# Optimization experiments

Hardware: AMD Instinct MI355X
Metric: run time of the kernel (lower is better)

The kernel has to match this reference:

```python
import jax, jax.numpy as jnp
import numpy as np

DEPTH = 9
SIGMA = 0.1
IN_SIGMA = 1.0
TOTAL_VARS = 2 ** DEPTH - 2  # 510 = sum of 2^(depth-d-1) for d in [0, depth-2]


def setup_inputs() -> dict:
    key = jax.random.key(0)
    N = 262144
    eps = jax.random.normal(key, (N, TOTAL_VARS), dtype=jnp.float32)
    return {"eps": eps, "N": N}


def reference(eps, N):
    # Collider binary tree sampling, vectorized per level.
    # Level d has 2^(DEPTH-d-1) variables; each variable's mean is the
    # join (sum) of a consecutive pair of parents from the previous level.
    outs = []
    offset = 0
    prev = None
    for d in range(DEPTH - 1):
        width = 2 ** (DEPTH - d - 1)
        e = jax.lax.dynamic_slice_in_dim(eps, offset, width, axis=1)  # [N, width]
        offset += width
        if d == 0:
            # root-level leaves: zero mean, in_sigma scale
            x = IN_SIGMA * e
        else:
            # join_link(parent_2k, parent_2k+1) = sum of adjacent pair
            m = prev[:, 0::2] + prev[:, 1::2]  # [N, width]
            x = m + SIGMA * e
        outs.append(x)
        prev = x
    # Flat level-major layout, same ordering as torch samples_list concatenated.
    return jnp.concatenate(outs, axis=1)  # [N, TOTAL_VARS]
```

## Files before the change

kernel.cpp:

```cpp
#include <hip/hip_runtime.h>


#define TOTAL_VARS 510
#define SIGMA 0.1f

__global__ __launch_bounds__(256) void collider_kernel(
    const float* __restrict__ eps,
    float* __restrict__ out,
    int N)
{
    const int wid  = (int)((blockIdx.x * blockDim.x + threadIdx.x) >> 6);
    const int lane = (int)(threadIdx.x & 63);
    if (wid >= N) return;

    const float* __restrict__ ep = eps + (size_t)wid * TOTAL_VARS;
    float* __restrict__ op = out + (size_t)wid * TOTAL_VARS;

    const float2 a01 = *reinterpret_cast<const float2*>(ep + 4 * lane);
    const float2 a23 = *reinterpret_cast<const float2*>(ep + 4 * lane + 2);
    *reinterpret_cast<float2*>(op + 4 * lane)     = a01;
    *reinterpret_cast<float2*>(op + 4 * lane + 2) = a23;

    const float2 e1 = *reinterpret_cast<const float2*>(ep + 256 + 2 * lane);
    const float x1a = a01.x + a01.y + SIGMA * e1.x;
    const float x1b = a23.x + a23.y + SIGMA * e1.y;
    float2 o1; o1.x = x1a; o1.y = x1b;
    *reinterpret_cast<float2*>(op + 256 + 2 * lane) = o1;

    const float e2 = ep[384 + lane];
    const float x2 = x1a + x1b + SIGMA * e2;
    op[384 + lane] = x2;

    float prev = x2;
#pragma unroll
    for (int d = 3; d < 8; ++d) {
        const int w   = 256 >> d;
        const int off = 512 - (512 >> d);
        const float a = __shfl(prev, 2 * lane);
        const float b = __shfl(prev, 2 * lane + 1);
        float e = 0.0f;
        if (lane < w) e = ep[off + lane];
        const float v = a + b + SIGMA * e;
        if (lane < w) op[off + lane] = v;
        prev = v;
    }
}

extern "C" void kernel_launch(void* const* d_in, const int* in_sizes, int n_in,
                              void* d_out, int out_size, void* d_ws, size_t ws_size,
                              hipStream_t stream) {
    const float* eps = (const float*)d_in[0];
    float* out = (float*)d_out;
    const int N = in_sizes[0] / TOTAL_VARS;

    const int threads = 256;
    const int rows_per_block = threads / 64;
    const int blocks = (N + rows_per_block - 1) / rows_per_block;
    collider_kernel<<<blocks, threads, 0, stream>>>(eps, out, N);
}
```

Baseline: 197.9 us.

## Stage 8-row blocks through LDS with coalesced float4 global loads and stores

Each block now copies 8 contiguous rows (4080 floats) from global memory into LDS using aligned float4 loads, computes the tree levels in LDS with two rows per wave, then writes the block back with float4 stores. This replaces the per-row float2 and scalar global accesses, which are misaligned because the row stride is 510 floats, with fully coalesced 16-byte transfers. In exchange it adds about 16KB of LDS per block, two barriers, and a launch that assumes N is divisible by 8 with no tail guard.

```diff
diff --git a/kernel.cpp b/kernel.cpp
--- a/kernel.cpp
+++ b/kernel.cpp
@@ -2,6 +2,9 @@
 
 
 #define TOTAL_VARS 510
+#define ROWS_PER_BLOCK 8
+#define BLOCK_FLOATS (ROWS_PER_BLOCK * TOTAL_VARS)
+#define BLOCK_F4     (BLOCK_FLOATS / 4)
 #define SIGMA 0.1f
 
 __global__ __launch_bounds__(256) void collider_kernel(
@@ -9,40 +12,61 @@
     float* __restrict__ out,
     int N)
 {
-    const int wid  = (int)((blockIdx.x * blockDim.x + threadIdx.x) >> 6);
-    const int lane = (int)(threadIdx.x & 63);
-    if (wid >= N) return;
+    __shared__ __align__(16) float lds[BLOCK_FLOATS];
 
-    const float* __restrict__ ep = eps + (size_t)wid * TOTAL_VARS;
-    float* __restrict__ op = out + (size_t)wid * TOTAL_VARS;
+    const int tid = (int)threadIdx.x;
+    const size_t base = (size_t)blockIdx.x * BLOCK_FLOATS;
 
-    const float2 a01 = *reinterpret_cast<const float2*>(ep + 4 * lane);
-    const float2 a23 = *reinterpret_cast<const float2*>(ep + 4 * lane + 2);
-    *reinterpret_cast<float2*>(op + 4 * lane)     = a01;
-    *reinterpret_cast<float2*>(op + 4 * lane + 2) = a23;
+    const float4* __restrict__ gin = reinterpret_cast<const float4*>(eps + base);
+    float4* l4 = reinterpret_cast<float4*>(lds);
+#pragma unroll
+    for (int i = 0; i < 4; ++i) {
+        const int idx = tid + i * 256;
+        if (idx < BLOCK_F4) l4[idx] = gin[idx];
+    }
+    __syncthreads();
 
-    const float2 e1 = *reinterpret_cast<const float2*>(ep + 256 + 2 * lane);
-    const float x1a = a01.x + a01.y + SIGMA * e1.x;
-    const float x1b = a23.x + a23.y + SIGMA * e1.y;
-    float2 o1; o1.x = x1a; o1.y = x1b;
-    *reinterpret_cast<float2*>(op + 256 + 2 * lane) = o1;
+    const int wave = tid >> 6;
+    const int lane = tid & 63;
 
-    const float e2 = ep[384 + lane];
-    const float x2 = x1a + x1b + SIGMA * e2;
-    op[384 + lane] = x2;
+#pragma unroll
+    for (int rr = 0; rr < 2; ++rr) {
+        float* row = lds + (wave * 2 + rr) * TOTAL_VARS;
 
-    float prev = x2;
+        const float2 a01 = *reinterpret_cast<const float2*>(row + 4 * lane);
+        const float2 a23 = *reinterpret_cast<const float2*>(row + 4 * lane + 2);
+
+        const float2 e1 = *reinterpret_cast<const float2*>(row + 256 + 2 * lane);
+        const float x1a = a01.x + a01.y + SIGMA * e1.x;
+        const float x1b = a23.x + a23.y + SIGMA * e1.y;
+        float2 o1; o1.x = x1a; o1.y = x1b;
+        *reinterpret_cast<float2*>(row + 256 + 2 * lane) = o1;
+
+        const float e2 = row[384 + lane];
+        const float x2 = x1a + x1b + SIGMA * e2;
+        row[384 + lane] = x2;
+
+        float prev = x2;
 #pragma unroll
-    for (int d = 3; d < 8; ++d) {
-        const int w   = 256 >> d;
-        const int off = 512 - (512 >> d);
-        const float a = __shfl(prev, 2 * lane);
-        const float b = __shfl(prev, 2 * lane + 1);
-        float e = 0.0f;
-        if (lane < w) e = ep[off + lane];
-        const float v = a + b + SIGMA * e;
-        if (lane < w) op[off + lane] = v;
-        prev = v;
+        for (int d = 3; d < 8; ++d) {
+            const int w   = 256 >> d;
+            const int off = 512 - (512 >> d);
+            const float a = __shfl(prev, 2 * lane);
+            const float b = __shfl(prev, 2 * lane + 1);
+            float e = 0.0f;
+            if (lane < w) e = row[off + lane];
+            const float v = a + b + SIGMA * e;
+            if (lane < w) row[off + lane] = v;
+            prev = v;
+        }
+    }
+    __syncthreads();
+
+    float4* __restrict__ gout = reinterpret_cast<float4*>(out + base);
+#pragma unroll
+    for (int i = 0; i < 4; ++i) {
+        const int idx = tid + i * 256;
+        if (idx < BLOCK_F4) gout[idx] = l4[idx];
     }
 }
 
@@ -53,8 +77,6 @@
     float* out = (float*)d_out;
     const int N = in_sizes[0] / TOTAL_VARS;
 
-    const int threads = 256;
-    const int rows_per_block = threads / 64;
-    const int blocks = (N + rows_per_block - 1) / rows_per_block;
-    collider_kernel<<<blocks, threads, 0, stream>>>(eps, out, N);
+    const int blocks = N / ROWS_PER_BLOCK;
+    collider_kernel<<<blocks, 256, 0, stream>>>(eps, out, N);
 }
```

After: 216.2 us. 9.3% more time.
